# Kernel optimization log

Measured on AMD Instinct MI355X. Metric: run time of the kernel, lower is better.

The kernel has to match this reference:

```python
import jax, jax.numpy as jnp
import numpy as np

IN_F = 4096
OUT_F = 4096
BATCH = 4
SEQ = 2048
QMAX = 16  # int4 levels


def setup_inputs() -> dict:
    key = jax.random.key(0)
    k_x, k_wq, k_s, k_z, k_t, k_m, k_b = jax.random.split(key, 7)
    x = jax.random.normal(k_x, (BATCH, SEQ, IN_F), dtype=jnp.float32)
    wq = jax.random.randint(k_wq, (OUT_F, IN_F), 0, QMAX, dtype=jnp.int32)
    qscale = jax.random.uniform(k_s, (OUT_F, 1), dtype=jnp.float32) * 0.01 + 1e-4
    qzero = jax.random.uniform(k_z, (OUT_F, 1), dtype=jnp.float32) * QMAX
    theta = jax.random.normal(k_t, (OUT_F, IN_F), dtype=jnp.float32) * 0.01
    mask = jax.random.randint(k_m, (OUT_F, IN_F), 0, 2, dtype=jnp.int32).astype(jnp.bool_)
    bias = jax.random.normal(k_b, (OUT_F,), dtype=jnp.float32) * 0.01
    return {"x": x, "wq": wq, "qscale": qscale, "qzero": qzero,
            "theta": theta, "mask": mask, "bias": bias}


def reference(x, wq, qscale, qzero, theta, mask, bias):
    # Per-output-channel int4 dequantization of active weights
    w_deq = (wq.astype(jnp.float32) - qzero) * qscale           # [out, in]
    m = mask.astype(jnp.float32)
    # Effective weight: active positions from dequantized W, pruned from theta
    w_eff = m * w_deq + (1.0 - m) * theta                        # [out, in]
    # F.linear: x @ W^T + b
    return jnp.einsum('bsi,oi->bso', x, w_eff) + bias
```

## Files before the change

kernel.cpp:

```cpp
#include <hip/hip_runtime.h>
#include <stdint.h>

typedef unsigned short u16;
typedef __bf16 bf16x8 __attribute__((ext_vector_type(8)));
typedef float f32x4 __attribute__((ext_vector_type(4)));

#define K_DIM 4096
#define N_OUT 4096
#define M_ROWS 8192


__device__ __forceinline__ u16 f2bf(float f) {
    uint32_t u = __builtin_bit_cast(uint32_t, f);
    u += 0x7fffu + ((u >> 16) & 1u);
    return (u16)(u >> 16);
}

__device__ __forceinline__ void gload_lds16(const void* g, void* l) {
    __builtin_amdgcn_global_load_lds(
        (const __attribute__((address_space(1))) void*)g,
        (__attribute__((address_space(3))) void*)l,
        16, 0, 0);
}

__device__ __forceinline__ int mask_is_int32(const void* maskp) {
    const uint32_t* u = (const uint32_t*)maskp;
    int ok = 1;
#pragma unroll
    for (int g = 0; g < 16; ++g) ok &= (u[g] <= 1u);
    return ok;
}


__global__ __launch_bounds__(256) void cvt_x_kernel(const float* __restrict__ x,
                                                    u16* __restrict__ xb) {
    size_t t = (size_t)blockIdx.x * 256 + threadIdx.x;
    const float4* p = (const float4*)x + t * 2;
    float4 a = p[0], b = p[1];
    union { u16 u[8]; uint4 v; } o;
    o.u[0] = f2bf(a.x); o.u[1] = f2bf(a.y); o.u[2] = f2bf(a.z); o.u[3] = f2bf(a.w);
    o.u[4] = f2bf(b.x); o.u[5] = f2bf(b.y); o.u[6] = f2bf(b.z); o.u[7] = f2bf(b.w);
    ((uint4*)xb)[t] = o.v;
}

__global__ __launch_bounds__(256) void build_w_kernel(const int* __restrict__ wq,
                                                      const float* __restrict__ qscale,
                                                      const float* __restrict__ qzero,
                                                      const float* __restrict__ theta,
                                                      const void* __restrict__ maskp,
                                                      u16* __restrict__ wb) {
    const int mi32 = mask_is_int32(maskp);
    size_t t = (size_t)blockIdx.x * 256 + threadIdx.x;
    size_t base = t * 8;
    int o = (int)(base >> 12);
    float s = qscale[o], z = qzero[o];

    int4 q0 = ((const int4*)wq)[t * 2];
    int4 q1 = ((const int4*)wq)[t * 2 + 1];
    float4 th0 = ((const float4*)theta)[t * 2];
    float4 th1 = ((const float4*)theta)[t * 2 + 1];

    int mv[8];
    if (mi32) {
        int4 m0 = ((const int4*)maskp)[t * 2];
        int4 m1 = ((const int4*)maskp)[t * 2 + 1];
        mv[0] = m0.x; mv[1] = m0.y; mv[2] = m0.z; mv[3] = m0.w;
        mv[4] = m1.x; mv[5] = m1.y; mv[6] = m1.z; mv[7] = m1.w;
    } else {
        uint2 mm = ((const uint2*)maskp)[t];
#pragma unroll
        for (int j = 0; j < 4; ++j) mv[j] = (mm.x >> (8 * j)) & 0xff;
#pragma unroll
        for (int j = 0; j < 4; ++j) mv[4 + j] = (mm.y >> (8 * j)) & 0xff;
    }

    float w[8];
    w[0] = mv[0] ? ((float)q0.x - z) * s : th0.x;
    w[1] = mv[1] ? ((float)q0.y - z) * s : th0.y;
    w[2] = mv[2] ? ((float)q0.z - z) * s : th0.z;
    w[3] = mv[3] ? ((float)q0.w - z) * s : th0.w;
    w[4] = mv[4] ? ((float)q1.x - z) * s : th1.x;
    w[5] = mv[5] ? ((float)q1.y - z) * s : th1.y;
    w[6] = mv[6] ? ((float)q1.z - z) * s : th1.z;
    w[7] = mv[7] ? ((float)q1.w - z) * s : th1.w;

    union { u16 u[8]; uint4 v; } ob;
#pragma unroll
    for (int j = 0; j < 8; ++j) ob.u[j] = f2bf(w[j]);
    ((uint4*)wb)[t] = ob.v;
}


__global__ __launch_bounds__(512, 2) void gemm8_kernel(const u16* __restrict__ xb,
                                                       const u16* __restrict__ wb,
                                                       const float* __restrict__ bias,
                                                       float* __restrict__ out) {
    __shared__ u16 lds[65536];

    const int tid = threadIdx.x;
    const int lane = tid & 63, wave = tid >> 6;
    const int wm = wave >> 2, wn = wave & 3;
    const int m0 = blockIdx.y * 256, n0 = blockIdx.x * 256;

    const int a_r = wm * 128 + (lane & 15);
    const int b_r = wn * 64 + (lane & 15);
    const int rslot = ((lane >> 4) ^ ((lane >> 1) & 3)) * 8;

    const int ch0 = wave * 2, ch1 = ch0 + 1;
    const int sRow = lane >> 2;
    const int sK = (((lane & 3) ^ ((lane >> 3) & 3)) * 8);
    const u16* gA0 = xb + (size_t)(m0 + ch0 * 16 + sRow) * K_DIM + sK;
    const u16* gA1 = xb + (size_t)(m0 + ch1 * 16 + sRow) * K_DIM + sK;
    const u16* gB0 = wb + (size_t)(n0 + ch0 * 16 + sRow) * K_DIM + sK;
    const u16* gB1 = wb + (size_t)(n0 + ch1 * 16 + sRow) * K_DIM + sK;

    f32x4 acc[8][4];
    const f32x4 zero = {0.f, 0.f, 0.f, 0.f};
#pragma unroll
    for (int m = 0; m < 8; ++m)
#pragma unroll
        for (int n = 0; n < 4; ++n) acc[m][n] = zero;

#define SA(BUF, KH, KT) { \
    const size_t kofs = (size_t)((KT) * 64 + (KH) * 32); \
    const int pl = ((BUF) * 2 + (KH)) * 8192; \
    gload_lds16(gA0 + kofs, &lds[pl + ch0 * 512]); \
    gload_lds16(gA1 + kofs, &lds[pl + ch1 * 512]); }
#define SB(BUF, KH, KT) { \
    const size_t kofs = (size_t)((KT) * 64 + (KH) * 32); \
    const int pl = 32768 + ((BUF) * 2 + (KH)) * 8192; \
    gload_lds16(gB0 + kofs, &lds[pl + ch0 * 512]); \
    gload_lds16(gB1 + kofs, &lds[pl + ch1 * 512]); }
#define DA(BUF, KS, MH) { \
    const int pa = ((BUF) * 2 + (KS)) * 8192 + (a_r + (MH) * 64) * 32 + rslot; \
    af[0] = *(const bf16x8*)&lds[pa]; \
    af[1] = *(const bf16x8*)&lds[pa + 512]; \
    af[2] = *(const bf16x8*)&lds[pa + 1024]; \
    af[3] = *(const bf16x8*)&lds[pa + 1536]; }
#define DB(BUF, KS) { \
    const int pb = 32768 + ((BUF) * 2 + (KS)) * 8192 + b_r * 32 + rslot; \
    bfr[0] = *(const bf16x8*)&lds[pb]; \
    bfr[1] = *(const bf16x8*)&lds[pb + 512]; \
    bfr[2] = *(const bf16x8*)&lds[pb + 1024]; \
    bfr[3] = *(const bf16x8*)&lds[pb + 1536]; }
#define MM(MH, M2) \
    acc[(MH)*4+(M2)][0] = __builtin_amdgcn_mfma_f32_16x16x32_bf16(af[M2], bfr[0], acc[(MH)*4+(M2)][0], 0, 0, 0); \
    acc[(MH)*4+(M2)][1] = __builtin_amdgcn_mfma_f32_16x16x32_bf16(af[M2], bfr[1], acc[(MH)*4+(M2)][1], 0, 0, 0); \
    acc[(MH)*4+(M2)][2] = __builtin_amdgcn_mfma_f32_16x16x32_bf16(af[M2], bfr[2], acc[(MH)*4+(M2)][2], 0, 0, 0); \
    acc[(MH)*4+(M2)][3] = __builtin_amdgcn_mfma_f32_16x16x32_bf16(af[M2], bfr[3], acc[(MH)*4+(M2)][3], 0, 0, 0);
#define MFMA16(MH) { \
    __builtin_amdgcn_s_setprio(1); \
    MM(MH, 0) MM(MH, 1) MM(MH, 2) MM(MH, 3) \
    __builtin_amdgcn_s_setprio(0); }
#define BAR() __builtin_amdgcn_s_barrier()
#define SCHED0() __builtin_amdgcn_sched_barrier(0)
#define VMW4() asm volatile("s_waitcnt vmcnt(4)" ::: "memory")

    SA(0, 0, 0); SB(0, 0, 0);
    SA(0, 1, 0); SB(0, 1, 0);
    SA(1, 0, 1); SB(1, 0, 1);
    asm volatile("s_waitcnt vmcnt(0)" ::: "memory");
    BAR();

#pragma unroll 1
    for (int j = 0; j < K_DIM / 128; ++j) {
        const int t1 = 2 * j + 1;
        const int t2 = (2 * j + 2) & 63;
        const int t3 = (2 * j + 3) & 63;
        bf16x8 af[4], bfr[4];
        DB(0, 0); DA(0, 0, 0); SA(1, 1, t1);
        BAR(); MFMA16(0); SCHED0(); BAR();
        DA(0, 0, 1); SB(1, 1, t1);
        BAR(); MFMA16(1); SCHED0(); BAR();
        DB(0, 1); DA(0, 1, 0); SA(0, 0, t2);
        BAR(); MFMA16(0); SCHED0(); BAR();
        DA(0, 1, 1); SB(0, 0, t2);
        BAR(); MFMA16(1); VMW4(); SCHED0(); BAR();
        DB(1, 0); DA(1, 0, 0); SA(0, 1, t2);
        BAR(); MFMA16(0); SCHED0(); BAR();
        DA(1, 0, 1); SB(0, 1, t2);
        BAR(); MFMA16(1); SCHED0(); BAR();
        DB(1, 1); DA(1, 1, 0); SA(1, 0, t3);
        BAR(); MFMA16(0); SCHED0(); BAR();
        DA(1, 1, 1); SB(1, 0, t3);
        BAR(); MFMA16(1); VMW4(); SCHED0(); BAR();
    }

    asm volatile("s_waitcnt vmcnt(0)" ::: "memory");

    const int rowBase = m0 + wm * 128 + ((lane >> 4) << 2);
    const int colBase = n0 + wn * 64 + (lane & 15);
#pragma unroll
    for (int n = 0; n < 4; ++n) {
        const int col = colBase + n * 16;
        const float bv = bias[col];
#pragma unroll
        for (int m = 0; m < 8; ++m) {
            const f32x4 v = acc[m][n];
            float* o = out + (size_t)(rowBase + m * 16) * N_OUT + col;
            o[0] = v[0] + bv;
            o[N_OUT] = v[1] + bv;
            o[2 * N_OUT] = v[2] + bv;
            o[3 * N_OUT] = v[3] + bv;
        }
    }
#undef SA
#undef SB
#undef DA
#undef DB
#undef MM
#undef MFMA16
#undef BAR
#undef SCHED0
#undef VMW4
}


__global__ __launch_bounds__(256) void fallback_kernel(const float* __restrict__ x,
                                                       const int* __restrict__ wq,
                                                       const float* __restrict__ qscale,
                                                       const float* __restrict__ qzero,
                                                       const float* __restrict__ theta,
                                                       const void* __restrict__ maskp,
                                                       const float* __restrict__ bias,
                                                       float* __restrict__ out) {
    __shared__ float xs[64][17];
    __shared__ float wsh[64][17];
    const int mi32 = mask_is_int32(maskp);
    const int n0 = blockIdx.x * 64, m0 = blockIdx.y * 64;
    const int t = threadIdx.x;
    const int tr = t >> 4, tc = t & 15;
    float acc[4][4] = {};

    for (int k0 = 0; k0 < K_DIM; k0 += 16) {
#pragma unroll
        for (int j = 0; j < 4; ++j) {
            int e = t * 4 + j;
            int r = e >> 4, c = e & 15;
            xs[r][c] = x[(size_t)(m0 + r) * K_DIM + k0 + c];
            int o = n0 + r;
            size_t idx = (size_t)o * K_DIM + k0 + c;
            float dq = ((float)wq[idx] - qzero[o]) * qscale[o];
            int mv = mi32 ? ((const int*)maskp)[idx] : ((const unsigned char*)maskp)[idx];
            wsh[r][c] = mv ? dq : theta[idx];
        }
        __syncthreads();
#pragma unroll
        for (int kk = 0; kk < 16; ++kk) {
            float a4[4], b4[4];
#pragma unroll
            for (int i = 0; i < 4; ++i) a4[i] = xs[tr * 4 + i][kk];
#pragma unroll
            for (int i = 0; i < 4; ++i) b4[i] = wsh[tc * 4 + i][kk];
#pragma unroll
            for (int i = 0; i < 4; ++i)
#pragma unroll
                for (int j = 0; j < 4; ++j) acc[i][j] += a4[i] * b4[j];
        }
        __syncthreads();
    }
#pragma unroll
    for (int i = 0; i < 4; ++i)
#pragma unroll
        for (int j = 0; j < 4; ++j)
            out[(size_t)(m0 + tr * 4 + i) * N_OUT + n0 + tc * 4 + j] =
                acc[i][j] + bias[n0 + tc * 4 + j];
}


extern "C" void kernel_launch(void* const* d_in, const int* in_sizes, int n_in,
                              void* d_out, int out_size, void* d_ws, size_t ws_size,
                              hipStream_t stream) {
    const float* x      = (const float*)d_in[0];
    const int*   wq     = (const int*)d_in[1];
    const float* qscale = (const float*)d_in[2];
    const float* qzero  = (const float*)d_in[3];
    const float* theta  = (const float*)d_in[4];
    const void*  mask   = d_in[5];
    const float* bias   = (const float*)d_in[6];
    float* out = (float*)d_out;

    const size_t xb_bytes = (size_t)M_ROWS * K_DIM * 2;
    const size_t wb_bytes = (size_t)N_OUT * K_DIM * 2;

    if (ws_size >= xb_bytes + wb_bytes) {
        u16* xb = (u16*)d_ws;
        u16* wb = (u16*)((char*)d_ws + xb_bytes);
        cvt_x_kernel<<<16384, 256, 0, stream>>>(x, xb);
        build_w_kernel<<<8192, 256, 0, stream>>>(wq, qscale, qzero, theta, mask, wb);
        dim3 grid(N_OUT / 256, M_ROWS / 256);
        gemm8_kernel<<<grid, 512, 0, stream>>>(xb, wb, bias, out);
    } else {
        dim3 grid(N_OUT / 64, M_ROWS / 64);
        fallback_kernel<<<grid, 256, 0, stream>>>(x, wq, qscale, qzero, theta, mask, bias, out);
    }
}
```

Measured before the change: 327.0 us.

## Double-buffer MFMA fragments in registers and drop one barrier per phase

The GEMM main loop now keeps two sets of A/B fragment registers. LDS reads for the next sub-tile are issued before the MFMA block that uses the current set, and the first fragments are loaded before the loop starts. Each phase now has one workgroup barrier instead of two, and the vmcnt wait runs every other phase. The goal is to hide LDS read latency behind matrix math and cut barrier stalls. The cost is higher register pressure, and the reordered waits and barriers could create LDS read/write races if the hazard analysis is wrong.

```diff
diff --git a/kernel.cpp b/kernel.cpp
--- a/kernel.cpp
+++ b/kernel.cpp
@@ -100,7 +100,8 @@
     const int tid = threadIdx.x;
     const int lane = tid & 63, wave = tid >> 6;
     const int wm = wave >> 2, wn = wave & 3;
-    const int m0 = blockIdx.y * 256, n0 = blockIdx.x * 256;
+    const int n0 = blockIdx.x * 256;
+    const int m0 = blockIdx.y * 256;
 
     const int a_r = wm * 128 + (lane & 15);
     const int b_r = wn * 64 + (lane & 15);
@@ -120,6 +121,9 @@
     for (int m = 0; m < 8; ++m)
 #pragma unroll
         for (int n = 0; n < 4; ++n) acc[m][n] = zero;
+
+    bf16x8 afA0, afA1, afA2, afA3, afB0, afB1, afB2, afB3;
+    bf16x8 bfA0, bfA1, bfA2, bfA3, bfB0, bfB1, bfB2, bfB3;
 
 #define SA(BUF, KH, KT) { \
     const size_t kofs = (size_t)((KT) * 64 + (KH) * 32); \
@@ -131,26 +135,37 @@
     const int pl = 32768 + ((BUF) * 2 + (KH)) * 8192; \
     gload_lds16(gB0 + kofs, &lds[pl + ch0 * 512]); \
     gload_lds16(gB1 + kofs, &lds[pl + ch1 * 512]); }
-#define DA(BUF, KS, MH) { \
+#define DAx(S, BUF, KS, MH) { \
     const int pa = ((BUF) * 2 + (KS)) * 8192 + (a_r + (MH) * 64) * 32 + rslot; \
-    af[0] = *(const bf16x8*)&lds[pa]; \
-    af[1] = *(const bf16x8*)&lds[pa + 512]; \
-    af[2] = *(const bf16x8*)&lds[pa + 1024]; \
-    af[3] = *(const bf16x8*)&lds[pa + 1536]; }
-#define DB(BUF, KS) { \
+    af##S##0 = *(const bf16x8*)&lds[pa]; \
+    af##S##1 = *(const bf16x8*)&lds[pa + 512]; \
+    af##S##2 = *(const bf16x8*)&lds[pa + 1024]; \
+    af##S##3 = *(const bf16x8*)&lds[pa + 1536]; }
+#define DBx(S, BUF, KS) { \
     const int pb = 32768 + ((BUF) * 2 + (KS)) * 8192 + b_r * 32 + rslot; \
-    bfr[0] = *(const bf16x8*)&lds[pb]; \
-    bfr[1] = *(const bf16x8*)&lds[pb + 512]; \
-    bfr[2] = *(const bf16x8*)&lds[pb + 1024]; \
-    bfr[3] = *(const bf16x8*)&lds[pb + 1536]; }
-#define MM(MH, M2) \
-    acc[(MH)*4+(M2)][0] = __builtin_amdgcn_mfma_f32_16x16x32_bf16(af[M2], bfr[0], acc[(MH)*4+(M2)][0], 0, 0, 0); \
-    acc[(MH)*4+(M2)][1] = __builtin_amdgcn_mfma_f32_16x16x32_bf16(af[M2], bfr[1], acc[(MH)*4+(M2)][1], 0, 0, 0); \
-    acc[(MH)*4+(M2)][2] = __builtin_amdgcn_mfma_f32_16x16x32_bf16(af[M2], bfr[2], acc[(MH)*4+(M2)][2], 0, 0, 0); \
-    acc[(MH)*4+(M2)][3] = __builtin_amdgcn_mfma_f32_16x16x32_bf16(af[M2], bfr[3], acc[(MH)*4+(M2)][3], 0, 0, 0);
-#define MFMA16(MH) { \
+    bf##S##0 = *(const bf16x8*)&lds[pb]; \
+    bf##S##1 = *(const bf16x8*)&lds[pb + 512]; \
+    bf##S##2 = *(const bf16x8*)&lds[pb + 1024]; \
+    bf##S##3 = *(const bf16x8*)&lds[pb + 1536]; }
+#define MF(A, B, C) __builtin_amdgcn_mfma_f32_16x16x32_bf16(A, B, C, 0, 0, 0)
+#define MFMA16(MH, AS, BS) { \
     __builtin_amdgcn_s_setprio(1); \
-    MM(MH, 0) MM(MH, 1) MM(MH, 2) MM(MH, 3) \
+    acc[(MH)*4+0][0] = MF(af##AS##0, bf##BS##0, acc[(MH)*4+0][0]); \
+    acc[(MH)*4+0][1] = MF(af##AS##0, bf##BS##1, acc[(MH)*4+0][1]); \
+    acc[(MH)*4+0][2] = MF(af##AS##0, bf##BS##2, acc[(MH)*4+0][2]); \
+    acc[(MH)*4+0][3] = MF(af##AS##0, bf##BS##3, acc[(MH)*4+0][3]); \
+    acc[(MH)*4+1][0] = MF(af##AS##1, bf##BS##0, acc[(MH)*4+1][0]); \
+    acc[(MH)*4+1][1] = MF(af##AS##1, bf##BS##1, acc[(MH)*4+1][1]); \
+    acc[(MH)*4+1][2] = MF(af##AS##1, bf##BS##2, acc[(MH)*4+1][2]); \
+    acc[(MH)*4+1][3] = MF(af##AS##1, bf##BS##3, acc[(MH)*4+1][3]); \
+    acc[(MH)*4+2][0] = MF(af##AS##2, bf##BS##0, acc[(MH)*4+2][0]); \
+    acc[(MH)*4+2][1] = MF(af##AS##2, bf##BS##1, acc[(MH)*4+2][1]); \
+    acc[(MH)*4+2][2] = MF(af##AS##2, bf##BS##2, acc[(MH)*4+2][2]); \
+    acc[(MH)*4+2][3] = MF(af##AS##2, bf##BS##3, acc[(MH)*4+2][3]); \
+    acc[(MH)*4+3][0] = MF(af##AS##3, bf##BS##0, acc[(MH)*4+3][0]); \
+    acc[(MH)*4+3][1] = MF(af##AS##3, bf##BS##1, acc[(MH)*4+3][1]); \
+    acc[(MH)*4+3][2] = MF(af##AS##3, bf##BS##2, acc[(MH)*4+3][2]); \
+    acc[(MH)*4+3][3] = MF(af##AS##3, bf##BS##3, acc[(MH)*4+3][3]); \
     __builtin_amdgcn_s_setprio(0); }
 #define BAR() __builtin_amdgcn_s_barrier()
 #define SCHED0() __builtin_amdgcn_sched_barrier(0)
@@ -161,29 +176,33 @@
     SA(1, 0, 1); SB(1, 0, 1);
     asm volatile("s_waitcnt vmcnt(0)" ::: "memory");
     BAR();
+    DBx(A, 0, 0); DAx(A, 0, 0, 0);
 
 #pragma unroll 1
     for (int j = 0; j < K_DIM / 128; ++j) {
         const int t1 = 2 * j + 1;
         const int t2 = (2 * j + 2) & 63;
         const int t3 = (2 * j + 3) & 63;
-        bf16x8 af[4], bfr[4];
-        DB(0, 0); DA(0, 0, 0); SA(1, 1, t1);
-        BAR(); MFMA16(0); SCHED0(); BAR();
-        DA(0, 0, 1); SB(1, 1, t1);
-        BAR(); MFMA16(1); SCHED0(); BAR();
-        DB(0, 1); DA(0, 1, 0); SA(0, 0, t2);
-        BAR(); MFMA16(0); SCHED0(); BAR();
-        DA(0, 1, 1); SB(0, 0, t2);
-        BAR(); MFMA16(1); VMW4(); SCHED0(); BAR();
-        DB(1, 0); DA(1, 0, 0); SA(0, 1, t2);
-        BAR(); MFMA16(0); SCHED0(); BAR();
-        DA(1, 0, 1); SB(0, 1, t2);
-        BAR(); MFMA16(1); SCHED0(); BAR();
-        DB(1, 1); DA(1, 1, 0); SA(1, 0, t3);
-        BAR(); MFMA16(0); SCHED0(); BAR();
-        DA(1, 1, 1); SB(1, 0, t3);
-        BAR(); MFMA16(1); VMW4(); SCHED0(); BAR();
+        VMW4();
+        DAx(B, 0, 0, 1); SA(1, 1, t1);
+        MFMA16(0, A, A); SCHED0(); BAR();
+        DAx(A, 0, 1, 0); DBx(B, 0, 1); SB(1, 1, t1);
+        MFMA16(1, B, A); SCHED0(); BAR();
+        VMW4();
+        DAx(B, 0, 1, 1); SA(0, 0, t2);
+        MFMA16(0, A, B); SCHED0(); BAR();
+        DAx(A, 1, 0, 0); DBx(A, 1, 0); SB(0, 0, t2);
+        MFMA16(1, B, B); SCHED0(); BAR();
+        VMW4();
+        DAx(B, 1, 0, 1); SA(0, 1, t2);
+        MFMA16(0, A, A); SCHED0(); BAR();
+        DAx(A, 1, 1, 0); DBx(B, 1, 1); SB(0, 1, t2);
+        MFMA16(1, B, A); SCHED0(); BAR();
+        VMW4();
+        DAx(B, 1, 1, 1); SA(1, 0, t3);
+        MFMA16(0, A, B); SCHED0(); BAR();
+        DAx(A, 0, 0, 0); DBx(A, 0, 0); SB(1, 0, t3);
+        MFMA16(1, B, B); SCHED0(); BAR();
     }
 
     asm volatile("s_waitcnt vmcnt(0)" ::: "memory");
@@ -206,9 +225,9 @@
     }
 #undef SA
 #undef SB
-#undef DA
-#undef DB
-#undef MM
+#undef DAx
+#undef DBx
+#undef MF
 #undef MFMA16
 #undef BAR
 #undef SCHED0
```

New measurement: 323.2 us. No clear change (-1.2%).

## Merge prep kernels and restructure GEMM main loop into four single-barrier phases

Applied to the files above, without the earlier changes.

Fuses the x bf16 conversion and the weight build into one prep kernel launch, which removes a launch and the gap between the two kernels. Rewrites the GEMM main loop so that each phase loads all eight A fragments and four B fragments, issues 32 MFMAs, then waits on vmcnt and issues the next A and B global-to-LDS loads together, with a single barrier per phase. This replaces eight half-phases that each had two barriers. The prologue now waits only for the first stage instead of all of them. The cost is more live fragment registers, which under launch bounds of 512 threads and 2 blocks could push register pressure toward spills. Load issue is also delayed until after the compute of each phase.

```diff
diff --git a/kernel.cpp b/kernel.cpp
--- a/kernel.cpp
+++ b/kernel.cpp
@@ -32,62 +32,63 @@
 }
 
 
-__global__ __launch_bounds__(256) void cvt_x_kernel(const float* __restrict__ x,
-                                                    u16* __restrict__ xb) {
-    size_t t = (size_t)blockIdx.x * 256 + threadIdx.x;
-    const float4* p = (const float4*)x + t * 2;
-    float4 a = p[0], b = p[1];
-    union { u16 u[8]; uint4 v; } o;
-    o.u[0] = f2bf(a.x); o.u[1] = f2bf(a.y); o.u[2] = f2bf(a.z); o.u[3] = f2bf(a.w);
-    o.u[4] = f2bf(b.x); o.u[5] = f2bf(b.y); o.u[6] = f2bf(b.z); o.u[7] = f2bf(b.w);
-    ((uint4*)xb)[t] = o.v;
-}
-
-__global__ __launch_bounds__(256) void build_w_kernel(const int* __restrict__ wq,
-                                                      const float* __restrict__ qscale,
-                                                      const float* __restrict__ qzero,
-                                                      const float* __restrict__ theta,
-                                                      const void* __restrict__ maskp,
-                                                      u16* __restrict__ wb) {
-    const int mi32 = mask_is_int32(maskp);
-    size_t t = (size_t)blockIdx.x * 256 + threadIdx.x;
-    size_t base = t * 8;
-    int o = (int)(base >> 12);
-    float s = qscale[o], z = qzero[o];
-
-    int4 q0 = ((const int4*)wq)[t * 2];
-    int4 q1 = ((const int4*)wq)[t * 2 + 1];
-    float4 th0 = ((const float4*)theta)[t * 2];
-    float4 th1 = ((const float4*)theta)[t * 2 + 1];
-
-    int mv[8];
-    if (mi32) {
-        int4 m0 = ((const int4*)maskp)[t * 2];
-        int4 m1 = ((const int4*)maskp)[t * 2 + 1];
-        mv[0] = m0.x; mv[1] = m0.y; mv[2] = m0.z; mv[3] = m0.w;
-        mv[4] = m1.x; mv[5] = m1.y; mv[6] = m1.z; mv[7] = m1.w;
+__global__ __launch_bounds__(256) void prep_kernel(const float* __restrict__ x,
+                                                   u16* __restrict__ xb,
+                                                   const int* __restrict__ wq,
+                                                   const float* __restrict__ qscale,
+                                                   const float* __restrict__ qzero,
+                                                   const float* __restrict__ theta,
+                                                   const void* __restrict__ maskp,
+                                                   u16* __restrict__ wb) {
+    if (blockIdx.x < 16384) {
+        size_t t = (size_t)blockIdx.x * 256 + threadIdx.x;
+        const float4* p = (const float4*)x + t * 2;
+        float4 a = p[0], b = p[1];
+        union { u16 u[8]; uint4 v; } o;
+        o.u[0] = f2bf(a.x); o.u[1] = f2bf(a.y); o.u[2] = f2bf(a.z); o.u[3] = f2bf(a.w);
+        o.u[4] = f2bf(b.x); o.u[5] = f2bf(b.y); o.u[6] = f2bf(b.z); o.u[7] = f2bf(b.w);
+        ((uint4*)xb)[t] = o.v;
     } else {
-        uint2 mm = ((const uint2*)maskp)[t];
-#pragma unroll
-        for (int j = 0; j < 4; ++j) mv[j] = (mm.x >> (8 * j)) & 0xff;
-#pragma unroll
-        for (int j = 0; j < 4; ++j) mv[4 + j] = (mm.y >> (8 * j)) & 0xff;
-    }
-
-    float w[8];
-    w[0] = mv[0] ? ((float)q0.x - z) * s : th0.x;
-    w[1] = mv[1] ? ((float)q0.y - z) * s : th0.y;
-    w[2] = mv[2] ? ((float)q0.z - z) * s : th0.z;
-    w[3] = mv[3] ? ((float)q0.w - z) * s : th0.w;
-    w[4] = mv[4] ? ((float)q1.x - z) * s : th1.x;
-    w[5] = mv[5] ? ((float)q1.y - z) * s : th1.y;
-    w[6] = mv[6] ? ((float)q1.z - z) * s : th1.z;
-    w[7] = mv[7] ? ((float)q1.w - z) * s : th1.w;
-
-    union { u16 u[8]; uint4 v; } ob;
-#pragma unroll
-    for (int j = 0; j < 8; ++j) ob.u[j] = f2bf(w[j]);
-    ((uint4*)wb)[t] = ob.v;
+        const int mi32 = mask_is_int32(maskp);
+        size_t t = (size_t)(blockIdx.x - 16384) * 256 + threadIdx.x;
+        size_t base = t * 8;
+        int o = (int)(base >> 12);
+        float s = qscale[o], z = qzero[o];
+
+        int4 q0 = ((const int4*)wq)[t * 2];
+        int4 q1 = ((const int4*)wq)[t * 2 + 1];
+        float4 th0 = ((const float4*)theta)[t * 2];
+        float4 th1 = ((const float4*)theta)[t * 2 + 1];
+
+        int mv[8];
+        if (mi32) {
+            int4 m0 = ((const int4*)maskp)[t * 2];
+            int4 m1 = ((const int4*)maskp)[t * 2 + 1];
+            mv[0] = m0.x; mv[1] = m0.y; mv[2] = m0.z; mv[3] = m0.w;
+            mv[4] = m1.x; mv[5] = m1.y; mv[6] = m1.z; mv[7] = m1.w;
+        } else {
+            uint2 mm = ((const uint2*)maskp)[t];
+#pragma unroll
+            for (int j = 0; j < 4; ++j) mv[j] = (mm.x >> (8 * j)) & 0xff;
+#pragma unroll
+            for (int j = 0; j < 4; ++j) mv[4 + j] = (mm.y >> (8 * j)) & 0xff;
+        }
+
+        float w[8];
+        w[0] = mv[0] ? ((float)q0.x - z) * s : th0.x;
+        w[1] = mv[1] ? ((float)q0.y - z) * s : th0.y;
+        w[2] = mv[2] ? ((float)q0.z - z) * s : th0.z;
+        w[3] = mv[3] ? ((float)q0.w - z) * s : th0.w;
+        w[4] = mv[4] ? ((float)q1.x - z) * s : th1.x;
+        w[5] = mv[5] ? ((float)q1.y - z) * s : th1.y;
+        w[6] = mv[6] ? ((float)q1.z - z) * s : th1.z;
+        w[7] = mv[7] ? ((float)q1.w - z) * s : th1.w;
+
+        union { u16 u[8]; uint4 v; } ob;
+#pragma unroll
+        for (int j = 0; j < 8; ++j) ob.u[j] = f2bf(w[j]);
+        ((uint4*)wb)[t] = ob.v;
+    }
 }
 
 
@@ -100,7 +101,8 @@
     const int tid = threadIdx.x;
     const int lane = tid & 63, wave = tid >> 6;
     const int wm = wave >> 2, wn = wave & 3;
-    const int m0 = blockIdx.y * 256, n0 = blockIdx.x * 256;
+    const int n0 = blockIdx.x * 256;
+    const int m0 = blockIdx.y * 256;
 
     const int a_r = wm * 128 + (lane & 15);
     const int b_r = wn * 64 + (lane & 15);
@@ -120,6 +122,8 @@
     for (int m = 0; m < 8; ++m)
 #pragma unroll
         for (int n = 0; n < 4; ++n) acc[m][n] = zero;
+
+    bf16x8 af0, af1, af2, af3, af4, af5, af6, af7, bf0, bf1, bf2, bf3;
 
 #define SA(BUF, KH, KT) { \
     const size_t kofs = (size_t)((KT) * 64 + (KH) * 32); \
@@ -131,35 +135,46 @@
     const int pl = 32768 + ((BUF) * 2 + (KH)) * 8192; \
     gload_lds16(gB0 + kofs, &lds[pl + ch0 * 512]); \
     gload_lds16(gB1 + kofs, &lds[pl + ch1 * 512]); }
-#define DA(BUF, KS, MH) { \
+#define DA(BUF, KS, MH, R0, R1, R2, R3) { \
     const int pa = ((BUF) * 2 + (KS)) * 8192 + (a_r + (MH) * 64) * 32 + rslot; \
-    af[0] = *(const bf16x8*)&lds[pa]; \
-    af[1] = *(const bf16x8*)&lds[pa + 512]; \
-    af[2] = *(const bf16x8*)&lds[pa + 1024]; \
-    af[3] = *(const bf16x8*)&lds[pa + 1536]; }
+    R0 = *(const bf16x8*)&lds[pa]; \
+    R1 = *(const bf16x8*)&lds[pa + 512]; \
+    R2 = *(const bf16x8*)&lds[pa + 1024]; \
+    R3 = *(const bf16x8*)&lds[pa + 1536]; }
 #define DB(BUF, KS) { \
     const int pb = 32768 + ((BUF) * 2 + (KS)) * 8192 + b_r * 32 + rslot; \
-    bfr[0] = *(const bf16x8*)&lds[pb]; \
-    bfr[1] = *(const bf16x8*)&lds[pb + 512]; \
-    bfr[2] = *(const bf16x8*)&lds[pb + 1024]; \
-    bfr[3] = *(const bf16x8*)&lds[pb + 1536]; }
-#define MM(MH, M2) \
-    acc[(MH)*4+(M2)][0] = __builtin_amdgcn_mfma_f32_16x16x32_bf16(af[M2], bfr[0], acc[(MH)*4+(M2)][0], 0, 0, 0); \
-    acc[(MH)*4+(M2)][1] = __builtin_amdgcn_mfma_f32_16x16x32_bf16(af[M2], bfr[1], acc[(MH)*4+(M2)][1], 0, 0, 0); \
-    acc[(MH)*4+(M2)][2] = __builtin_amdgcn_mfma_f32_16x16x32_bf16(af[M2], bfr[2], acc[(MH)*4+(M2)][2], 0, 0, 0); \
-    acc[(MH)*4+(M2)][3] = __builtin_amdgcn_mfma_f32_16x16x32_bf16(af[M2], bfr[3], acc[(MH)*4+(M2)][3], 0, 0, 0);
-#define MFMA16(MH) { \
+    bf0 = *(const bf16x8*)&lds[pb]; \
+    bf1 = *(const bf16x8*)&lds[pb + 512]; \
+    bf2 = *(const bf16x8*)&lds[pb + 1024]; \
+    bf3 = *(const bf16x8*)&lds[pb + 1536]; }
+#define MF(A, B, C) __builtin_amdgcn_mfma_f32_16x16x32_bf16(A, B, C, 0, 0, 0)
+#define MROW(M, AF) { \
+    acc[M][0] = MF(AF, bf0, acc[M][0]); \
+    acc[M][1] = MF(AF, bf1, acc[M][1]); \
+    acc[M][2] = MF(AF, bf2, acc[M][2]); \
+    acc[M][3] = MF(AF, bf3, acc[M][3]); }
+#define MFMA32() { \
     __builtin_amdgcn_s_setprio(1); \
-    MM(MH, 0) MM(MH, 1) MM(MH, 2) MM(MH, 3) \
+    MROW(0, af0) MROW(1, af1) MROW(2, af2) MROW(3, af3) \
+    MROW(4, af4) MROW(5, af5) MROW(6, af6) MROW(7, af7) \
     __builtin_amdgcn_s_setprio(0); }
 #define BAR() __builtin_amdgcn_s_barrier()
 #define SCHED0() __builtin_amdgcn_sched_barrier(0)
 #define VMW4() asm volatile("s_waitcnt vmcnt(4)" ::: "memory")
 
+#define PHASE(BUF, KS, STB, STK, STT) { \
+    DA(BUF, KS, 0, af0, af1, af2, af3); \
+    DB(BUF, KS); \
+    DA(BUF, KS, 1, af4, af5, af6, af7); \
+    MFMA32(); \
+    VMW4(); \
+    SA(STB, STK, STT); SB(STB, STK, STT); \
+    SCHED0(); BAR(); }
+
     SA(0, 0, 0); SB(0, 0, 0);
     SA(0, 1, 0); SB(0, 1, 0);
     SA(1, 0, 1); SB(1, 0, 1);
-    asm volatile("s_waitcnt vmcnt(0)" ::: "memory");
+    asm volatile("s_waitcnt vmcnt(8)" ::: "memory");
     BAR();
 
 #pragma unroll 1
@@ -167,23 +182,10 @@
         const int t1 = 2 * j + 1;
         const int t2 = (2 * j + 2) & 63;
         const int t3 = (2 * j + 3) & 63;
-        bf16x8 af[4], bfr[4];
-        DB(0, 0); DA(0, 0, 0); SA(1, 1, t1);
-        BAR(); MFMA16(0); SCHED0(); BAR();
-        DA(0, 0, 1); SB(1, 1, t1);
-        BAR(); MFMA16(1); SCHED0(); BAR();
-        DB(0, 1); DA(0, 1, 0); SA(0, 0, t2);
-        BAR(); MFMA16(0); SCHED0(); BAR();
-        DA(0, 1, 1); SB(0, 0, t2);
-        BAR(); MFMA16(1); VMW4(); SCHED0(); BAR();
-        DB(1, 0); DA(1, 0, 0); SA(0, 1, t2);
-        BAR(); MFMA16(0); SCHED0(); BAR();
-        DA(1, 0, 1); SB(0, 1, t2);
-        BAR(); MFMA16(1); SCHED0(); BAR();
-        DB(1, 1); DA(1, 1, 0); SA(1, 0, t3);
-        BAR(); MFMA16(0); SCHED0(); BAR();
-        DA(1, 1, 1); SB(1, 0, t3);
-        BAR(); MFMA16(1); VMW4(); SCHED0(); BAR();
+        PHASE(0, 0, 1, 1, t1);
+        PHASE(0, 1, 0, 0, t2);
+        PHASE(1, 0, 0, 1, t2);
+        PHASE(1, 1, 1, 0, t3);
     }
 
     asm volatile("s_waitcnt vmcnt(0)" ::: "memory");
@@ -208,11 +210,13 @@
 #undef SB
 #undef DA
 #undef DB
-#undef MM
-#undef MFMA16
+#undef MF
+#undef MROW
+#undef MFMA32
 #undef BAR
 #undef SCHED0
 #undef VMW4
+#undef PHASE
 }
 
 
@@ -286,8 +290,7 @@
     if (ws_size >= xb_bytes + wb_bytes) {
         u16* xb = (u16*)d_ws;
         u16* wb = (u16*)((char*)d_ws + xb_bytes);
-        cvt_x_kernel<<<16384, 256, 0, stream>>>(x, xb);
-        build_w_kernel<<<8192, 256, 0, stream>>>(wq, qscale, qzero, theta, mask, wb);
+        prep_kernel<<<24576, 256, 0, stream>>>(x, xb, wq, qscale, qzero, theta, mask, wb);
         dim3 grid(N_OUT / 256, M_ROWS / 256);
         gemm8_kernel<<<grid, 512, 0, stream>>>(xb, wb, bias, out);
     } else {
```

New measurement: 331.0 us. About the same (+1.2%).
